# Kernel tuning notes

Measured on AMD Instinct MI355X. Metric: run time of the kernel, lower is better.

Reference implementation:

```python
import jax, jax.numpy as jnp
import numpy as np
from jax import lax

SPIKE_RATE = 100.0
TIME_STEPS = 100
ADAPT_FACTOR = 0.95
REFRACTORY = 2.0
N_NEURONS = 256


def setup_inputs() -> dict:
    key = jax.random.key(0)
    x = jax.random.normal(jax.random.fold_in(key, 1), (32, 64), dtype=jnp.float32)
    centers = jnp.linspace(-1.0, 1.0, N_NEURONS).astype(jnp.float32)
    widths = jnp.full((N_NEURONS,), 0.2, dtype=jnp.float32)
    adaptation_state = jnp.ones((N_NEURONS,), dtype=jnp.float32)
    refractory_state = jnp.zeros((N_NEURONS,), dtype=jnp.float32)
    return {
        "x": x,
        "centers": centers,
        "widths": widths,
        "adaptation_state": adaptation_state,
        "refractory_state": refractory_state,
        "seed": 0,
    }


def reference(x, centers, widths, adaptation_state, refractory_state, seed):
    # x: [B, F]; centers/widths/states: [N]
    # Gaussian tuning-curve response: [B, F, N]
    d = x[:, :, None] - centers[None, None, :]
    response = jnp.exp(-(d * d) / (2.0 * widths * widths))
    # adaptation applied once with the initial buffer state (as in torch source)
    response = response * adaptation_state[None, None, :]
    spike_prob = response * (SPIKE_RATE / 1000.0)

    base_key = jax.random.key(seed)

    def step(carry, t):
        ref, adapt = carry  # each [N]
        k = jax.random.fold_in(base_key, t)
        r = jax.random.uniform(k, spike_prob.shape, dtype=spike_prob.dtype)
        can_spike = (ref == 0).astype(spike_prob.dtype)  # [N]
        spike_t = (r < spike_prob).astype(spike_prob.dtype) * can_spike[None, None, :]
        ref = jnp.maximum(ref - 1.0, 0.0)
        occurred = spike_t.sum(axis=(0, 1)) > 0  # [N]
        ref = ref + occurred.astype(ref.dtype) * REFRACTORY
        adapt = adapt * jnp.where(occurred, ADAPT_FACTOR, 1.0)
        return (ref, adapt), spike_t

    (_, _), spikes = lax.scan(step, (refractory_state, adaptation_state),
                              jnp.arange(TIME_STEPS))
    # spikes: [T, B, F, N] -> [B, F, N, T] to match torch.stack(..., dim=-1)
    return jnp.moveaxis(spikes, 0, -1)
```

## Files before the change

kernel.cpp:

```cpp
#include <hip/hip_runtime.h>
#include <stdint.h>

typedef unsigned long long u64;
typedef unsigned int u32;
typedef float f32x4 __attribute__((ext_vector_type(4)));

#define T_STEPS 100
#define NNEUR 256
#define NBF 2048
#define NELEM (NBF * NNEUR)

__device__ __forceinline__ void tf2x32(u32 k0, u32 k1, u32& x0, u32& x1) {
  u32 k2 = k0 ^ k1 ^ 0x1BD11BDAu;
  x0 += k0; x1 += k1;
#define TFR(r) { x0 += x1; x1 = (x1 << (r)) | (x1 >> (32 - (r))); x1 ^= x0; }
  TFR(13) TFR(15) TFR(26) TFR(6)
  x0 += k1; x1 += k2 + 1u;
  TFR(17) TFR(29) TFR(16) TFR(24)
  x0 += k2; x1 += k0 + 2u;
  TFR(13) TFR(15) TFR(26) TFR(6)
  x0 += k0; x1 += k1 + 3u;
  TFR(17) TFR(29) TFR(16) TFR(24)
  x0 += k1; x1 += k2 + 4u;
  TFR(13) TFR(15) TFR(26) TFR(6)
  x0 += k2; x1 += k0 + 5u;
#undef TFR
}

__device__ __forceinline__ u32 rotl32(u32 x, int r) {
  return __builtin_amdgcn_alignbit(x, x, 32 - r);
}

__global__ void __launch_bounds__(256) kern_p(
    const float* __restrict__ x, const float* __restrict__ c,
    const float* __restrict__ w, const float* __restrict__ a,
    u32* __restrict__ thr9, u32* __restrict__ occ32) {
  int idx = blockIdx.x * 256 + threadIdx.x;
  int n = idx & 255, bf = idx >> 8;
  float d = x[bf] - c[n];
  float denom = (2.0f * w[n]) * w[n];
  float q = -(d * d) / denom;
  float e = (float)exp((double)q);
  float p = (e * a[n]) * 0.1f;
  thr9[idx] = ((u32)ceilf(p * 8388608.0f)) << 9;
  if (blockIdx.x == 0 && threadIdx.x < 200) {
    ((uint4*)occ32)[threadIdx.x] = make_uint4(0u, 0u, 0u, 0u);
  }
}

__global__ void __launch_bounds__(256, 8) kern_bits3(
    const u32* __restrict__ thr9,
    const int* __restrict__ seedp,
    u32* __restrict__ cmp32,
    u32* __restrict__ occ32) {
  const int t = blockIdx.x;
  const int g = blockIdx.y;
  const int tid = threadIdx.x;
  const int hoct = tid & 15;
  const int bfl = tid >> 4;
  const int bf = g * 16 + bfl;
  const u32 seed = (u32)__builtin_amdgcn_readfirstlane((int)seedp[0]);

  u32 K0 = 0u, K1 = (u32)t;
  tf2x32(0u, seed, K0, K1);
  const u32 K2 = K0 ^ K1 ^ 0x1BD11BDAu;
  const u32 I10 = K1;
  const u32 I11 = K2 + 1u;
  const u32 I20 = K2;
  const u32 I21 = K0 + 2u;
  const u32 I30 = K0;
  const u32 I31 = K1 + 3u;
  const u32 I40 = K1;
  const u32 I41 = K2 + 4u;
  const u32 I50 = K2;
  const u32 I51 = K0 + 5u;

  const u32 base_i = (u32)(bf * 256 + hoct * 16);

  u32 th[16];
  const uint4* tp = (const uint4*)(thr9 + base_i);
#pragma unroll
  for (int q = 0; q < 4; ++q) {
    uint4 v = tp[q];
    th[4*q] = v.x; th[4*q+1] = v.y; th[4*q+2] = v.z; th[4*q+3] = v.w;
  }

  const u32 x1base = base_i + K1;
  const u32 x0base = x1base + K0;
  u32 word = 0u;
#pragma unroll
  for (int k = 15; k >= 0; --k) {
    u32 x1 = x1base + (u32)k;
    u32 x0 = x0base + (u32)k;
    x1 = rotl32(x1, 13); x1 ^= x0;
#define QR(r) { x0 += x1; x1 = rotl32(x1, r); x1 ^= x0; }
    QR(15) QR(26) QR(6)
    x0 += I10; x1 += I11;
    QR(17) QR(29) QR(16) QR(24)
    x0 += I20; x1 += I21;
    QR(13) QR(15) QR(26) QR(6)
    x0 += I30; x1 += I31;
    QR(17) QR(29) QR(16) QR(24)
    x0 += I40; x1 += I41;
    QR(13) QR(15) QR(26) QR(6)
    x0 += I50; x1 += I51;
#undef QR
    word = (word << 1) | ((x0 ^ x1) < th[k] ? 1u : 0u);
  }

  u32 partner = (u32)__shfl_xor((int)word, 1, 64);
  if (!(hoct & 1)) {
    u32 word32 = word | (partner << 16);
    cmp32[(u32)bf * (T_STEPS * 8) + (u32)t * 8 + (hoct >> 1)] = word32;
  }

  u32 o = word;
  o |= (u32)__shfl_xor((int)o, 16, 64);
  o |= (u32)__shfl_xor((int)o, 32, 64);
  u32 op = (u32)__shfl_xor((int)o, 1, 64);
  if ((tid & 63) < 16 && !(hoct & 1)) {
    atomicOr(&occ32[t * 8 + (hoct >> 1)], o | (op << 16));
  }
}

__global__ void __launch_bounds__(256) kern_out3(
    const u32* __restrict__ cmp32,
    const u32* __restrict__ occ32,
    const float* __restrict__ ref0,
    float* __restrict__ out) {
  __shared__ u32 s_occ[T_STEPS * 8];
  __shared__ u32 s_can[T_STEPS * 8];
  __shared__ u32 s[8 * T_STEPS];
  const int bf = blockIdx.x;
  const int tid = threadIdx.x;

  uint4 myc = make_uint4(0u, 0u, 0u, 0u);
  if (tid < 200) {
    myc = ((const uint4*)(cmp32 + (u64)bf * (T_STEPS * 8)))[tid];
    ((uint4*)s_occ)[tid] = ((const uint4*)occ32)[tid];
  }
  __syncthreads();

  {
    const int n = tid, lane = n & 63, v = n >> 6;
    float ref = ref0[n];
    for (int t = 0; t < T_STEPS; ++t) {
      bool can = (ref == 0.0f);
      u64 cm = __ballot(can);
      if (lane == 0) {
        s_can[t * 8 + v * 2]     = (u32)cm;
        s_can[t * 8 + v * 2 + 1] = (u32)(cm >> 32);
      }
      bool occb = (s_occ[t * 8 + (n >> 5)] >> (n & 31)) & 1u;
      bool occurred = can && occb;
      ref = fmaxf(ref - 1.0f, 0.0f) + (occurred ? 2.0f : 0.0f);
    }
  }
  __syncthreads();

  if (tid < 200) {
    const int t = tid >> 1, w0 = (tid & 1) * 4;
    const u32* mp = (const u32*)&myc;
#pragma unroll
    for (int j = 0; j < 4; ++j) {
      s[(w0 + j) * T_STEPS + t] = mp[j] & s_can[t * 8 + w0 + j];
    }
  }
  __syncthreads();

  f32x4* outv = (f32x4*)(out + (u64)bf * (NNEUR * T_STEPS));
#pragma unroll
  for (int kk = 0; kk < 25; ++kk) {
    int q = tid + 256 * kk;
    int e = q * 4;
    int n = e / 100;
    int t0 = e - n * 100;
    int bit = n & 31;
    uint4 wv = *(const uint4*)&s[(n >> 5) * T_STEPS + t0];
    f32x4 val;
    val[0] = (float)((wv.x >> bit) & 1u);
    val[1] = (float)((wv.y >> bit) & 1u);
    val[2] = (float)((wv.z >> bit) & 1u);
    val[3] = (float)((wv.w >> bit) & 1u);
    __builtin_nontemporal_store(val, &outv[q]);
  }
}

__global__ void __launch_bounds__(256) kern_bits_fb(
    const float* __restrict__ x, const float* __restrict__ c,
    const float* __restrict__ w, const float* __restrict__ a,
    const int* __restrict__ seedp,
    float* __restrict__ outf,
    u64* __restrict__ occ64) {
  const int t = blockIdx.x;
  const int chunk = blockIdx.y;
  const int lane = threadIdx.x & 63;
  const int v = threadIdx.x >> 6;
  const int n = v * 64 + lane;
  const u32 seed = (u32)seedp[0];
  u32 kt0 = 0u, kt1 = (u32)t;
  tf2x32(0u, seed, kt0, kt1);
  float cn = c[n], wn = w[n], an = a[n];
  bool occ = false;
  for (int j = 0; j < 64; ++j) {
    int bf = chunk * 64 + j;
    u32 i = (u32)(bf * 256 + n);
    u32 b0 = 0u, b1 = i;
    tf2x32(kt0, kt1, b0, b1);
    u32 bits = b0 ^ b1;
    float r = __uint_as_float((bits >> 9) | 0x3F800000u) - 1.0f;
    float d = x[bf] - cn;
    float denom = (2.0f * wn) * wn;
    float q = -(d * d) / denom;
    float pv = ((float)exp((double)q) * an) * 0.1f;
    bool cm = r < pv;
    occ |= cm;
    outf[(u64)bf * (NNEUR * T_STEPS) + (u64)n * T_STEPS + t] = cm ? 1.0f : 0.0f;
  }
  u64 om = __ballot(occ);
  if (lane == 0) atomicOr(&occ64[t * 4 + v], om);
}

__global__ void __launch_bounds__(256) kern_rec(
    const float* __restrict__ ref0,
    const u64* __restrict__ occ64,
    u64* __restrict__ can64) {
  int n = threadIdx.x;
  int lane = n & 63, v = n >> 6;
  float ref = ref0[n];
  for (int t = 0; t < T_STEPS; ++t) {
    bool can = (ref == 0.0f);
    u64 cm = __ballot(can);
    if (lane == 0) can64[t * 4 + v] = cm;
    bool occb = (occ64[t * 4 + v] >> lane) & 1ull;
    bool occurred = can && occb;
    ref = fmaxf(ref - 1.0f, 0.0f) + (occurred ? 2.0f : 0.0f);
  }
}

__global__ void __launch_bounds__(256) kern_mask(
    const u32* __restrict__ can32, float* __restrict__ out) {
  u64 q = (u64)blockIdx.x * 256 + threadIdx.x;
  float4* ov = (float4*)out;
  float4 vx = ov[q];
  u32 local = (u32)((q * 4) % (NNEUR * T_STEPS));
  float* vp = (float*)&vx;
#pragma unroll
  for (int j = 0; j < 4; ++j) {
    u32 le = local + j;
    u32 n = le / 100;
    u32 t = le - n * 100;
    u32 bit = (can32[t * 8 + (n >> 5)] >> (n & 31)) & 1u;
    vp[j] = bit ? vp[j] : 0.0f;
  }
  ov[q] = vx;
}

extern "C" void kernel_launch(void* const* d_in, const int* in_sizes, int n_in,
                              void* d_out, int out_size, void* d_ws, size_t ws_size,
                              hipStream_t stream) {
  const float* x  = (const float*)d_in[0];
  const float* c  = (const float*)d_in[1];
  const float* w  = (const float*)d_in[2];
  const float* a  = (const float*)d_in[3];
  const float* r0 = (const float*)d_in[4];
  const int* seed = (const int*)d_in[5];
  float* out = (float*)d_out;

  const size_t P_BYTES   = (size_t)NELEM * 4;
  const size_t CMP_BYTES = (size_t)NBF * T_STEPS * 4 * 8;
  const size_t OCC_BYTES = (size_t)T_STEPS * 4 * 8;
  const bool full = ws_size >= P_BYTES + CMP_BYTES + 2 * OCC_BYTES;

  uint8_t* wsb = (uint8_t*)d_ws;

  if (full) {
    u32* thr   = (u32*)wsb;
    u32* cmp   = (u32*)(wsb + P_BYTES);
    u32* occ   = (u32*)(wsb + P_BYTES + CMP_BYTES);
    kern_p<<<NELEM / 256, 256, 0, stream>>>(x, c, w, a, thr, occ);
    kern_bits3<<<dim3(T_STEPS, 128), 256, 0, stream>>>(thr, seed, cmp, occ);
    kern_out3<<<NBF, 256, 0, stream>>>(cmp, occ, r0, out);
  } else {
    u64* occ = (u64*)wsb;
    u64* can = (u64*)(wsb + OCC_BYTES);
    hipMemsetAsync(occ, 0, OCC_BYTES, stream);
    kern_bits_fb<<<dim3(T_STEPS, 32), 256, 0, stream>>>(x, c, w, a, seed, out, occ);
    kern_rec<<<1, 256, 0, stream>>>(r0, occ, can);
    kern_mask<<<(out_size / 4) / 256, 256, 0, stream>>>((const u32*)can, out);
  }
}
```

Before: 336.0 us.

## Fuse threshold, RNG and output kernels into one cooperative grid-synced kernel

Replaces the three-kernel pipeline (threshold, RNG bits, output expansion) with a single cooperative kernel of 1600 persistent blocks that uses grid-wide syncs between phases. Each block processes several RNG tiles, then redundantly recomputes the refractory recurrence in shared memory and writes several output rows. The aim is to remove kernel-launch gaps and inter-kernel drain. In exchange it depends on cooperative-launch residency, repeats the serial recurrence in every block, and drops the small-workspace fallback path.

```diff
diff --git a/kernel.cpp b/kernel.cpp
--- a/kernel.cpp
+++ b/kernel.cpp
@@ -1,4 +1,5 @@
 #include <hip/hip_runtime.h>
+#include <hip/hip_cooperative_groups.h>
 #include <stdint.h>
 
 typedef unsigned long long u64;
@@ -9,6 +10,9 @@
 #define NNEUR 256
 #define NBF 2048
 #define NELEM (NBF * NNEUR)
+#define COOP_BLOCKS 1600
+#define TILES 12800
+#define TILES_PER_BLK 8
 
 __device__ __forceinline__ void tf2x32(u32 k0, u32 k1, u32& x0, u32& x1) {
   u32 k2 = k0 ^ k1 ^ 0x1BD11BDAu;
@@ -31,6 +35,164 @@
   return __builtin_amdgcn_alignbit(x, x, 32 - r);
 }
 
+__global__ void __launch_bounds__(256, 8) kern_fused(
+    const float* __restrict__ x, const float* __restrict__ c,
+    const float* __restrict__ w, const float* __restrict__ a,
+    const float* __restrict__ ref0, const int* __restrict__ seedp,
+    u32* __restrict__ thr9, u32* __restrict__ cmp32,
+    u32* __restrict__ occ32, float* __restrict__ out) {
+  __shared__ u32 s_occ[T_STEPS * 8];
+  __shared__ u32 s_can[T_STEPS * 8];
+  __shared__ u32 s[8 * T_STEPS];
+  const int bid = blockIdx.x;
+  const int tid = threadIdx.x;
+
+  for (int idx = bid * 256 + tid; idx < NELEM; idx += COOP_BLOCKS * 256) {
+    int n = idx & 255, bf = idx >> 8;
+    float d = x[bf] - c[n];
+    float denom = (2.0f * w[n]) * w[n];
+    float q = -(d * d) / denom;
+    float e = (float)exp((double)q);
+    float p = (e * a[n]) * 0.1f;
+    thr9[idx] = ((u32)ceilf(p * 8388608.0f)) << 9;
+  }
+  if (bid == 0 && tid < 200) {
+    ((uint4*)occ32)[tid] = make_uint4(0u, 0u, 0u, 0u);
+  }
+
+  cooperative_groups::this_grid().sync();
+
+  {
+    const int hoct = tid & 15;
+    const int bfl = tid >> 4;
+    const u32 seed = (u32)__builtin_amdgcn_readfirstlane((int)seedp[0]);
+#pragma unroll 1
+    for (int it = 0; it < TILES_PER_BLK; ++it) {
+      const int tile = bid * TILES_PER_BLK + it;
+      const int t = tile >> 7;
+      const int g = tile & 127;
+      const int bf = g * 16 + bfl;
+
+      u32 K0 = 0u, K1 = (u32)t;
+      tf2x32(0u, seed, K0, K1);
+      const u32 K2 = K0 ^ K1 ^ 0x1BD11BDAu;
+      const u32 I10 = K1;
+      const u32 I11 = K2 + 1u;
+      const u32 I20 = K2;
+      const u32 I21 = K0 + 2u;
+      const u32 I30 = K0;
+      const u32 I31 = K1 + 3u;
+      const u32 I40 = K1;
+      const u32 I41 = K2 + 4u;
+      const u32 I50 = K2;
+      const u32 I51 = K0 + 5u;
+
+      const u32 base_i = (u32)(bf * 256 + hoct * 16);
+
+      u32 th[16];
+      const uint4* tp = (const uint4*)(thr9 + base_i);
+#pragma unroll
+      for (int q = 0; q < 4; ++q) {
+        uint4 v = tp[q];
+        th[4*q] = v.x; th[4*q+1] = v.y; th[4*q+2] = v.z; th[4*q+3] = v.w;
+      }
+
+      const u32 x1base = base_i + K1;
+      const u32 x0base = x1base + K0;
+      u32 word = 0u;
+#pragma unroll
+      for (int k = 15; k >= 0; --k) {
+        u32 x1 = x1base + (u32)k;
+        u32 x0 = x0base + (u32)k;
+        x1 = rotl32(x1, 13); x1 ^= x0;
+#define QR(r) { x0 += x1; x1 = rotl32(x1, r); x1 ^= x0; }
+        QR(15) QR(26) QR(6)
+        x0 += I10; x1 += I11;
+        QR(17) QR(29) QR(16) QR(24)
+        x0 += I20; x1 += I21;
+        QR(13) QR(15) QR(26) QR(6)
+        x0 += I30; x1 += I31;
+        QR(17) QR(29) QR(16) QR(24)
+        x0 += I40; x1 += I41;
+        QR(13) QR(15) QR(26) QR(6)
+        x0 += I50; x1 += I51;
+#undef QR
+        word = (word << 1) | ((x0 ^ x1) < th[k] ? 1u : 0u);
+      }
+
+      u32 partner = (u32)__shfl_xor((int)word, 1, 64);
+      if (!(hoct & 1)) {
+        cmp32[(u32)bf * (T_STEPS * 8) + (u32)t * 8 + (hoct >> 1)] =
+            word | (partner << 16);
+      }
+
+      u32 o = word;
+      o |= (u32)__shfl_xor((int)o, 16, 64);
+      o |= (u32)__shfl_xor((int)o, 32, 64);
+      u32 op = (u32)__shfl_xor((int)o, 1, 64);
+      if ((tid & 63) < 16 && !(hoct & 1)) {
+        atomicOr(&occ32[t * 8 + (hoct >> 1)], o | (op << 16));
+      }
+    }
+  }
+
+  cooperative_groups::this_grid().sync();
+
+  if (tid < 200) ((uint4*)s_occ)[tid] = ((const uint4*)occ32)[tid];
+  __syncthreads();
+
+  {
+    const int n = tid, lane = n & 63, v = n >> 6;
+    float ref = ref0[n];
+    for (int t = 0; t < T_STEPS; ++t) {
+      bool can = (ref == 0.0f);
+      u64 cm = __ballot(can);
+      if (lane == 0) {
+        s_can[t * 8 + v * 2]     = (u32)cm;
+        s_can[t * 8 + v * 2 + 1] = (u32)(cm >> 32);
+      }
+      bool occb = (s_occ[t * 8 + (n >> 5)] >> (n & 31)) & 1u;
+      bool occurred = can && occb;
+      ref = fmaxf(ref - 1.0f, 0.0f) + (occurred ? 2.0f : 0.0f);
+    }
+  }
+  __syncthreads();
+
+#pragma unroll 1
+  for (int bf = bid; bf < NBF; bf += COOP_BLOCKS) {
+    uint4 myc = make_uint4(0u, 0u, 0u, 0u);
+    if (tid < 200) myc = ((const uint4*)(cmp32 + (u64)bf * (T_STEPS * 8)))[tid];
+
+    if (tid < 200) {
+      const int t = tid >> 1, w0 = (tid & 1) * 4;
+      const u32* mp = (const u32*)&myc;
+#pragma unroll
+      for (int j = 0; j < 4; ++j) {
+        s[(w0 + j) * T_STEPS + t] = mp[j] & s_can[t * 8 + w0 + j];
+      }
+    }
+    __syncthreads();
+
+    f32x4* outv = (f32x4*)(out + (u64)bf * (NNEUR * T_STEPS));
+#pragma unroll
+    for (int kk = 0; kk < 25; ++kk) {
+      int q = tid + 256 * kk;
+      int e = q * 4;
+      int n = e / 100;
+      int t0 = e - n * 100;
+      int bit = n & 31;
+      uint4 wv = *(const uint4*)&s[(n >> 5) * T_STEPS + t0];
+      f32x4 val;
+      val[0] = (float)((wv.x >> bit) & 1u);
+      val[1] = (float)((wv.y >> bit) & 1u);
+      val[2] = (float)((wv.z >> bit) & 1u);
+      val[3] = (float)((wv.w >> bit) & 1u);
+      __builtin_nontemporal_store(val, &outv[q]);
+    }
+    __syncthreads();
+  }
+}
+
 __global__ void __launch_bounds__(256) kern_p(
     const float* __restrict__ x, const float* __restrict__ c,
     const float* __restrict__ w, const float* __restrict__ a,
@@ -76,7 +238,6 @@
   const u32 I51 = K0 + 5u;
 
   const u32 base_i = (u32)(bf * 256 + hoct * 16);
-
   u32 th[16];
   const uint4* tp = (const uint4*)(thr9 + base_i);
 #pragma unroll
@@ -110,10 +271,9 @@
 
   u32 partner = (u32)__shfl_xor((int)word, 1, 64);
   if (!(hoct & 1)) {
-    u32 word32 = word | (partner << 16);
-    cmp32[(u32)bf * (T_STEPS * 8) + (u32)t * 8 + (hoct >> 1)] = word32;
-  }
-
+    cmp32[(u32)bf * (T_STEPS * 8) + (u32)t * 8 + (hoct >> 1)] =
+        word | (partner << 16);
+  }
   u32 o = word;
   o |= (u32)__shfl_xor((int)o, 16, 64);
   o |= (u32)__shfl_xor((int)o, 32, 64);
@@ -186,76 +346,6 @@
   }
 }
 
-__global__ void __launch_bounds__(256) kern_bits_fb(
-    const float* __restrict__ x, const float* __restrict__ c,
-    const float* __restrict__ w, const float* __restrict__ a,
-    const int* __restrict__ seedp,
-    float* __restrict__ outf,
-    u64* __restrict__ occ64) {
-  const int t = blockIdx.x;
-  const int chunk = blockIdx.y;
-  const int lane = threadIdx.x & 63;
-  const int v = threadIdx.x >> 6;
-  const int n = v * 64 + lane;
-  const u32 seed = (u32)seedp[0];
-  u32 kt0 = 0u, kt1 = (u32)t;
-  tf2x32(0u, seed, kt0, kt1);
-  float cn = c[n], wn = w[n], an = a[n];
-  bool occ = false;
-  for (int j = 0; j < 64; ++j) {
-    int bf = chunk * 64 + j;
-    u32 i = (u32)(bf * 256 + n);
-    u32 b0 = 0u, b1 = i;
-    tf2x32(kt0, kt1, b0, b1);
-    u32 bits = b0 ^ b1;
-    float r = __uint_as_float((bits >> 9) | 0x3F800000u) - 1.0f;
-    float d = x[bf] - cn;
-    float denom = (2.0f * wn) * wn;
-    float q = -(d * d) / denom;
-    float pv = ((float)exp((double)q) * an) * 0.1f;
-    bool cm = r < pv;
-    occ |= cm;
-    outf[(u64)bf * (NNEUR * T_STEPS) + (u64)n * T_STEPS + t] = cm ? 1.0f : 0.0f;
-  }
-  u64 om = __ballot(occ);
-  if (lane == 0) atomicOr(&occ64[t * 4 + v], om);
-}
-
-__global__ void __launch_bounds__(256) kern_rec(
-    const float* __restrict__ ref0,
-    const u64* __restrict__ occ64,
-    u64* __restrict__ can64) {
-  int n = threadIdx.x;
-  int lane = n & 63, v = n >> 6;
-  float ref = ref0[n];
-  for (int t = 0; t < T_STEPS; ++t) {
-    bool can = (ref == 0.0f);
-    u64 cm = __ballot(can);
-    if (lane == 0) can64[t * 4 + v] = cm;
-    bool occb = (occ64[t * 4 + v] >> lane) & 1ull;
-    bool occurred = can && occb;
-    ref = fmaxf(ref - 1.0f, 0.0f) + (occurred ? 2.0f : 0.0f);
-  }
-}
-
-__global__ void __launch_bounds__(256) kern_mask(
-    const u32* __restrict__ can32, float* __restrict__ out) {
-  u64 q = (u64)blockIdx.x * 256 + threadIdx.x;
-  float4* ov = (float4*)out;
-  float4 vx = ov[q];
-  u32 local = (u32)((q * 4) % (NNEUR * T_STEPS));
-  float* vp = (float*)&vx;
-#pragma unroll
-  for (int j = 0; j < 4; ++j) {
-    u32 le = local + j;
-    u32 n = le / 100;
-    u32 t = le - n * 100;
-    u32 bit = (can32[t * 8 + (n >> 5)] >> (n & 31)) & 1u;
-    vp[j] = bit ? vp[j] : 0.0f;
-  }
-  ov[q] = vx;
-}
-
 extern "C" void kernel_launch(void* const* d_in, const int* in_sizes, int n_in,
                               void* d_out, int out_size, void* d_ws, size_t ws_size,
                               hipStream_t stream) {
@@ -270,23 +360,21 @@
   const size_t P_BYTES   = (size_t)NELEM * 4;
   const size_t CMP_BYTES = (size_t)NBF * T_STEPS * 4 * 8;
   const size_t OCC_BYTES = (size_t)T_STEPS * 4 * 8;
-  const bool full = ws_size >= P_BYTES + CMP_BYTES + 2 * OCC_BYTES;
 
   uint8_t* wsb = (uint8_t*)d_ws;
-
-  if (full) {
-    u32* thr   = (u32*)wsb;
-    u32* cmp   = (u32*)(wsb + P_BYTES);
-    u32* occ   = (u32*)(wsb + P_BYTES + CMP_BYTES);
+  u32* thr = (u32*)wsb;
+  u32* cmp = (u32*)(wsb + P_BYTES);
+  u32* occ = (u32*)(wsb + P_BYTES + CMP_BYTES);
+  (void)OCC_BYTES;
+
+  void* args[] = {(void*)&x, (void*)&c, (void*)&w, (void*)&a, (void*)&r0,
+                  (void*)&seed, (void*)&thr, (void*)&cmp, (void*)&occ,
+                  (void*)&out};
+  hipError_t err = hipLaunchCooperativeKernel(
+      (const void*)kern_fused, dim3(COOP_BLOCKS), dim3(256), args, 0, stream);
+  if (err != hipSuccess) {
     kern_p<<<NELEM / 256, 256, 0, stream>>>(x, c, w, a, thr, occ);
     kern_bits3<<<dim3(T_STEPS, 128), 256, 0, stream>>>(thr, seed, cmp, occ);
     kern_out3<<<NBF, 256, 0, stream>>>(cmp, occ, r0, out);
-  } else {
-    u64* occ = (u64*)wsb;
-    u64* can = (u64*)(wsb + OCC_BYTES);
-    hipMemsetAsync(occ, 0, OCC_BYTES, stream);
-    kern_bits_fb<<<dim3(T_STEPS, 32), 256, 0, stream>>>(x, c, w, a, seed, out, occ);
-    kern_rec<<<1, 256, 0, stream>>>(r0, occ, can);
-    kern_mask<<<(out_size / 4) / 256, 256, 0, stream>>>((const u32*)can, out);
-  }
-}
+  }
+}
```

After: 765.3 us. +127.8%, slower.
